# Kernel optimization log

Measured on AMD Instinct MI355X. Metric: run time of the kernel, lower is better.

Reference implementation:

```python
import jax, jax.numpy as jnp
import numpy as np
import math

T, R, H = 3, 5, 8
IN = 256
OUT = 256
DK = OUT // H
N, E, MAXLEN = 30000, 200000, 240
EPS = 1e-5


def _layernorm(x):
    mu = jnp.mean(x, -1, keepdims=True)
    var = jnp.mean((x - mu) ** 2, -1, keepdims=True)
    return (x - mu) / jnp.sqrt(var + EPS)


def _rte_table():
    # fixed sinusoid table from RelTemporalEncoding (non-trainable)
    pos = np.arange(MAXLEN, dtype=np.float32)[:, None]
    div = np.exp(np.arange(0, IN, 2, dtype=np.float32) * -(math.log(10000.0) / IN))
    emb = np.zeros((MAXLEN, IN), dtype=np.float32)
    emb[:, 0::2] = np.sin(pos * div) / math.sqrt(IN)
    emb[:, 1::2] = np.cos(pos * div) / math.sqrt(IN)
    return jnp.asarray(emb)


def setup_inputs():
    key = jax.random.key(0)
    ks = jax.random.split(key, 16)
    g = lambda k, shape, s: jax.random.normal(k, shape, jnp.float32) * s
    inp = {}
    inp['node_inp'] = g(ks[0], (N, IN), 1.0)
    inp['Wk'] = g(ks[1], (T, IN, OUT), 0.02)
    inp['bk'] = jnp.zeros((T, OUT), jnp.float32)
    inp['Wq'] = g(ks[2], (T, IN, OUT), 0.02)
    inp['bq'] = jnp.zeros((T, OUT), jnp.float32)
    inp['Wv'] = g(ks[3], (T, IN, OUT), 0.02)
    inp['bv'] = jnp.zeros((T, OUT), jnp.float32)
    inp['Wa'] = g(ks[4], (T, OUT, OUT), 0.02)
    inp['ba'] = jnp.zeros((T, OUT), jnp.float32)
    inp['ln_g'] = jnp.ones((T, OUT), jnp.float32)
    inp['ln_b'] = jnp.zeros((T, OUT), jnp.float32)
    inp['rel_pri'] = jnp.ones((R, H), jnp.float32)
    inp['rel_att'] = g(ks[5], (R, H, DK, DK), 1.0 / math.sqrt(DK))
    inp['rel_msg'] = g(ks[6], (R, H, DK, DK), 1.0 / math.sqrt(DK))
    inp['skip'] = jnp.ones((T,), jnp.float32)
    inp['rte_W'] = g(ks[7], (IN, IN), 0.02)
    inp['rte_b'] = jnp.zeros((IN,), jnp.float32)
    inp['rte_emb'] = _rte_table()
    inp['node_type'] = jax.random.randint(ks[8], (N,), 0, T)
    inp['edge_index'] = jax.random.randint(ks[9], (2, E), 0, N)
    inp['edge_type'] = jax.random.randint(ks[10], (E,), 0, R)
    inp['edge_time'] = jax.random.randint(ks[11], (E,), 0, MAXLEN)
    return inp


def _forward(node_inp, Wk, bk, Wq, bq, Wv, bv, Wa, ba, ln_g, ln_b,
             rel_pri, rel_att, rel_msg, skip, rte_W, rte_b, rte_emb,
             node_type, edge_index, edge_type, edge_time):
    src, dst = edge_index[0], edge_index[1]  # j (source), i (target)
    nidx = jnp.arange(N)
    # per-type node projections, then pick each node's own type row
    q_node = (jnp.einsum('ni,tio->tno', node_inp, Wq) + bq[:, None, :])[node_type, nidx]
    k_node = (jnp.einsum('ni,tio->tno', node_inp, Wk) + bk[:, None, :])[node_type, nidx]
    v_node = (jnp.einsum('ni,tio->tno', node_inp, Wv) + bv[:, None, :])[node_type, nidx]
    # k_linear(x + rte) = k_linear(x) + rte @ Wk  -> precompute tiny [T, MAXLEN, OUT] tables
    rte_vec = rte_emb @ rte_W.T + rte_b           # [MAXLEN, IN], lin(emb(t))
    rte_k = jnp.einsum('mi,tio->tmo', rte_vec, Wk)
    rte_v = jnp.einsum('mi,tio->tmo', rte_vec, Wv)
    st = node_type[src]
    k_e = (k_node[src] + rte_k[st, edge_time]).reshape(E, H, DK)
    v_e = (v_node[src] + rte_v[st, edge_time]).reshape(E, H, DK)
    q_e = q_node[dst].reshape(E, H, DK)
    # relation-specific bilinear transforms (static small loop over R)
    k_t = jnp.zeros_like(k_e)
    v_t = jnp.zeros_like(v_e)
    for r in range(R):
        m = (edge_type == r)[:, None, None]
        k_t = jnp.where(m, jnp.einsum('ehd,hdf->ehf', k_e, rel_att[r]), k_t)
        v_t = jnp.where(m, jnp.einsum('ehd,hdf->ehf', v_e, rel_msg[r]), v_t)
    logit = jnp.sum(q_e * k_t, -1) * rel_pri[edge_type] / math.sqrt(DK)  # [E, H]
    # segment softmax grouped by target node id
    mx = jax.ops.segment_max(logit, dst, num_segments=N)
    ex = jnp.exp(logit - mx[dst])
    den = jax.ops.segment_sum(ex, dst, num_segments=N)
    att = ex / den[dst]
    msg = (v_t * att[:, :, None]).reshape(E, OUT)
    aggr = jax.ops.segment_sum(msg, dst, num_segments=N)  # [N, OUT]
    # target-specific aggregation, gated skip (dropout is eval no-op)
    trans = (jnp.einsum('no,tof->tnf', aggr, Wa) + ba[:, None, :])[node_type, nidx]
    alpha = jax.nn.sigmoid(skip)[node_type][:, None]
    mixed = trans * alpha + node_inp * (1.0 - alpha)
    return _layernorm(mixed) * ln_g[node_type] + ln_b[node_type]


def reference(node_inp, node_type, edge_index, edge_type, edge_time,
              Wk, bk, Wq, bq, Wv, bv, Wa, ba, ln_g, ln_b,
              rel_pri, rel_att, rel_msg, skip, rte_W, rte_b, rte_emb):
    return _forward(node_inp, Wk, bk, Wq, bq, Wv, bv, Wa, ba, ln_g, ln_b,
                    rel_pri, rel_att, rel_msg, skip, rte_W, rte_b, rte_emb,
                    node_type, edge_index, edge_type, edge_time)
```

## Files before the change

kernel.cpp:

```cpp
#include <hip/hip_runtime.h>
#include <hip/hip_bf16.h>
#include <math.h>

#define NN 30000
#define NE 200000
#define NT 3
#define NR 5
#define NH 8
#define DIM 256
#define ML 240
#define EPSF 1e-5f

typedef __attribute__((ext_vector_type(8))) short short8v;
typedef __attribute__((ext_vector_type(4))) float f32x4;

__device__ __forceinline__ unsigned fkey(float f){
    unsigned b = __float_as_uint(f);
    return (b & 0x80000000u) ? ~b : (b | 0x80000000u);
}
__device__ __forceinline__ float funkey(unsigned u){
    return __uint_as_float((u & 0x80000000u) ? (u & 0x7fffffffu) : ~u);
}
__device__ __forceinline__ unsigned short f2bf(float f){
    unsigned b = __float_as_uint(f);
    unsigned r = (b + 0x7FFFu + ((b >> 16) & 1u)) >> 16;
    return (unsigned short)r;
}

__global__ void k_cvt(const float* __restrict__ in, unsigned short* __restrict__ out){
    int idx = blockIdx.x*256 + threadIdx.x;
    const float4* s = reinterpret_cast<const float4*>(in + (size_t)idx*8);
    float4 a = s[0], b = s[1];
    unsigned short t[8];
    t[0]=f2bf(a.x); t[1]=f2bf(a.y); t[2]=f2bf(a.z); t[3]=f2bf(a.w);
    t[4]=f2bf(b.x); t[5]=f2bf(b.y); t[6]=f2bf(b.z); t[7]=f2bf(b.w);
    *reinterpret_cast<uint4*>(out + (size_t)idx*8) = *reinterpret_cast<uint4*>(t);
}

__global__ __launch_bounds__(256) void k_cvt_w(const float* __restrict__ W,
                                               unsigned short* __restrict__ Wt){
    __shared__ float S[64][65];
    int t = blockIdx.z;
    int i0 = blockIdx.x * 64, o0 = blockIdx.y * 64;
    int th = threadIdx.x;
    int r = th >> 2, c0 = (th & 3) * 16;
    const float* src = W + (size_t)t*65536 + (size_t)(i0 + r)*256 + o0 + c0;
    #pragma unroll
    for (int j = 0; j < 16; j += 4){
        float4 v = *reinterpret_cast<const float4*>(src + j);
        S[r][c0 + j + 0] = v.x; S[r][c0 + j + 1] = v.y;
        S[r][c0 + j + 2] = v.z; S[r][c0 + j + 3] = v.w;
    }
    __syncthreads();
    unsigned short tmp[16];
    #pragma unroll
    for (int j = 0; j < 16; j++) tmp[j] = f2bf(S[c0 + j][r]);
    unsigned short* dst = Wt + (size_t)t*65536 + (size_t)(o0 + r)*256 + i0 + c0;
    *reinterpret_cast<uint4*>(dst)     = *reinterpret_cast<uint4*>(tmp);
    *reinterpret_cast<uint4*>(dst + 8) = *reinterpret_cast<uint4*>(tmp + 8);
}

__global__ void k_rtevec(const float* __restrict__ emb, const float* __restrict__ W,
                         const float* __restrict__ b, float* __restrict__ out){
    __shared__ float se[DIM];
    int m = blockIdx.x, i = threadIdx.x;
    se[i] = emb[m*DIM + i];
    __syncthreads();
    const float* wr = W + i*DIM;
    float acc = 0.f;
    #pragma unroll 8
    for (int j = 0; j < DIM; j += 4){
        float4 w = *reinterpret_cast<const float4*>(wr + j);
        acc += se[j]*w.x + se[j+1]*w.y + se[j+2]*w.z + se[j+3]*w.w;
    }
    out[m*DIM + i] = acc + b[i];
}

__global__ void k_rtekv(const float* __restrict__ rvec, const float* __restrict__ Wk,
                        const float* __restrict__ Wv, float* __restrict__ rk,
                        float* __restrict__ rv){
    __shared__ float sv[DIM];
    int m = blockIdx.x, t = blockIdx.y, o = threadIdx.x;
    sv[o] = rvec[m*DIM + o];
    __syncthreads();
    const float* wk = Wk + (size_t)t*DIM*DIM;
    const float* wv = Wv + (size_t)t*DIM*DIM;
    float ak = 0.f, av = 0.f;
    #pragma unroll 4
    for (int i = 0; i < DIM; i++){
        float s = sv[i];
        ak += s * wk[i*DIM + o];
        av += s * wv[i*DIM + o];
    }
    rk[(t*ML+m)*DIM + o] = ak;
    rv[(t*ML+m)*DIM + o] = av;
}

__global__ void k_bucket(const int* __restrict__ ntype, const int* __restrict__ etype,
                         int* __restrict__ ncnt, int* __restrict__ nlist,
                         int* __restrict__ ecnt, int* __restrict__ elist){
    __shared__ int lc[8];
    __shared__ int lb[8];
    int tid = threadIdx.x;
    if (tid < 8) lc[tid] = 0;
    __syncthreads();
    int idx = blockIdx.x*256 + tid;
    int key = -1, lpos = 0;
    if (idx < NN){
        key = ntype[idx];
        lpos = atomicAdd(&lc[key], 1);
    } else if (idx < NN + NE){
        key = NT + etype[idx - NN];
        lpos = atomicAdd(&lc[key], 1);
    }
    __syncthreads();
    if (tid < 8 && lc[tid] > 0){
        lb[tid] = atomicAdd(tid < NT ? &ncnt[tid] : &ecnt[tid - NT], lc[tid]);
    }
    __syncthreads();
    if (idx < NN){
        nlist[key*NN + lb[key] + lpos] = idx;
    } else if (idx < NN + NE){
        elist[(key - NT)*NE + lb[key] + lpos] = idx - NN;
    }
}

__global__ __launch_bounds__(256) void k_projM(const unsigned short* __restrict__ Xb,
        const int* __restrict__ nlist, const int* __restrict__ ncnt,
        const unsigned short* __restrict__ Wt, const float* __restrict__ bias,
        float* __restrict__ Y){
    __shared__ unsigned short As[128*40];
    __shared__ unsigned short Bs[128*40];
    int t = blockIdx.z;
    int cnt = ncnt[t];
    int m0 = blockIdx.x * 128;
    if (m0 >= cnt) return;
    int o0 = blockIdx.y * 128;
    int th = threadIdx.x;
    const unsigned short* Wtt = Wt + (size_t)t*65536;

    int srow = th >> 1, shalf = th & 1;
    int arow = m0 + srow;
    int anode = (arow < cnt) ? nlist[t*NN + arow] : nlist[t*NN];
    const unsigned short* agp = Xb + (size_t)anode*256 + shalf*16;
    const unsigned short* bgp = Wtt + (size_t)(o0 + srow)*256 + shalf*16;
    uint4* alp = reinterpret_cast<uint4*>(&As[srow*40 + shalf*16]);
    uint4* blp = reinterpret_cast<uint4*>(&Bs[srow*40 + shalf*16]);

    int l = th & 63, w = th >> 6;
    int wm = w >> 1, wn = w & 1;
    int lrow = l & 15, kc = l >> 4;

    f32x4 acc[4][4];
    #pragma unroll
    for (int i = 0; i < 4; i++)
        #pragma unroll
        for (int j = 0; j < 4; j++) acc[i][j] = (f32x4){0.f,0.f,0.f,0.f};

    for (int k0 = 0; k0 < 256; k0 += 32){
        uint4 ga0 = *reinterpret_cast<const uint4*>(agp + k0);
        uint4 ga1 = *reinterpret_cast<const uint4*>(agp + k0 + 8);
        uint4 gb0 = *reinterpret_cast<const uint4*>(bgp + k0);
        uint4 gb1 = *reinterpret_cast<const uint4*>(bgp + k0 + 8);
        __syncthreads();
        alp[0] = ga0; alp[1] = ga1;
        blp[0] = gb0; blp[1] = gb1;
        __syncthreads();
        short8v a[4], b[4];
        #pragma unroll
        for (int mi = 0; mi < 4; mi++)
            a[mi] = *reinterpret_cast<const short8v*>(&As[(wm*64 + mi*16 + lrow)*40 + kc*8]);
        #pragma unroll
        for (int ni = 0; ni < 4; ni++)
            b[ni] = *reinterpret_cast<const short8v*>(&Bs[(wn*64 + ni*16 + lrow)*40 + kc*8]);
        #pragma unroll
        for (int mi = 0; mi < 4; mi++)
            #pragma unroll
            for (int ni = 0; ni < 4; ni++)
                acc[mi][ni] = __builtin_amdgcn_mfma_f32_16x16x32_bf16(a[mi], b[ni], acc[mi][ni], 0, 0, 0);
    }

    float bv[4];
    #pragma unroll
    for (int ni = 0; ni < 4; ni++)
        bv[ni] = bias[t*256 + o0 + wn*64 + ni*16 + (l & 15)];
    #pragma unroll
    for (int mi = 0; mi < 4; mi++){
        #pragma unroll
        for (int j = 0; j < 4; j++){
            int grow = m0 + wm*64 + mi*16 + (l >> 4)*4 + j;
            if (grow < cnt){
                int node = nlist[t*NN + grow];
                float* yp = Y + (size_t)node*256 + o0 + wn*64 + (l & 15);
                #pragma unroll
                for (int ni = 0; ni < 4; ni++)
                    yp[ni*16] = acc[mi][ni][j] + bv[ni];
            }
        }
    }
}

__global__ __launch_bounds__(256) void k_passA(const float* __restrict__ qn,
        const float* __restrict__ kn, const float* __restrict__ rk,
        const int* __restrict__ elist, const int* __restrict__ ecnt,
        const int* __restrict__ esrc, const int* __restrict__ edst,
        const int* __restrict__ etime, const int* __restrict__ ntype,
        const float* __restrict__ rel_att, const float* __restrict__ rel_pri,
        float* __restrict__ logit, unsigned* __restrict__ mx){
    __shared__ int s_src[64], s_dst[64], s_tm[64], s_st[64], s_eid[64];
    __shared__ float ke[64][36], qe[64][36];
    int r = blockIdx.y;
    int cnt = ecnt[r];
    int e0 = blockIdx.x * 64;
    if (e0 >= cnt) return;
    int nE = min(64, cnt - e0);
    int tid = threadIdx.x;
    if (tid < 64){
        int e = elist[r*NE + e0 + (tid < nE ? tid : 0)];
        int sj = esrc[e];
        s_eid[tid] = e; s_src[tid] = sj; s_dst[tid] = edst[e];
        s_tm[tid] = etime[e]; s_st[tid] = ntype[sj];
    }
    __syncthreads();
    int f = tid & 31, mg = tid >> 5;
    const float inv = 0.17677669529663687f;
    for (int h = 0; h < NH; h++){
        #pragma unroll
        for (int u = 0; u < 2; u++){
            int fi = tid + u*256;
            int m = fi >> 3, c4 = (fi & 7) * 4;
            float4 kv = *reinterpret_cast<const float4*>(kn + (size_t)s_src[m]*DIM + h*32 + c4);
            float4 rvv = *reinterpret_cast<const float4*>(rk + (size_t)(s_st[m]*ML + s_tm[m])*DIM + h*32 + c4);
            float4 qv = *reinterpret_cast<const float4*>(qn + (size_t)s_dst[m]*DIM + h*32 + c4);
            kv.x += rvv.x; kv.y += rvv.y; kv.z += rvv.z; kv.w += rvv.w;
            *reinterpret_cast<float4*>(&ke[m][c4]) = kv;
            *reinterpret_cast<float4*>(&qe[m][c4]) = qv;
        }
        __syncthreads();
        float rf[32];
        const float* relb = rel_att + (size_t)(r*NH + h)*1024;
        #pragma unroll
        for (int d = 0; d < 32; d++) rf[d] = relb[d*32 + f];
        float pri = rel_pri[r*NH + h] * inv;
        #pragma unroll
        for (int mi = 0; mi < 8; mi++){
            int m = mg*8 + mi;
            float acc = 0.f;
            #pragma unroll
            for (int d4 = 0; d4 < 8; d4++){
                float4 k4 = *reinterpret_cast<const float4*>(&ke[m][d4*4]);
                acc += k4.x*rf[d4*4] + k4.y*rf[d4*4+1] + k4.z*rf[d4*4+2] + k4.w*rf[d4*4+3];
            }
            float v = acc * qe[m][f];
            v += __shfl_xor(v, 1);
            v += __shfl_xor(v, 2);
            v += __shfl_xor(v, 4);
            v += __shfl_xor(v, 8);
            v += __shfl_xor(v, 16);
            if (f == 0 && m < nE){
                float lv = v * pri;
                logit[(size_t)s_eid[m]*NH + h] = lv;
                atomicMax(&mx[s_dst[m]*NH + h], fkey(lv));
            }
        }
        __syncthreads();
    }
}

__global__ __launch_bounds__(256) void k_passB(const float* __restrict__ vn,
        const float* __restrict__ rv, const int* __restrict__ elist,
        const int* __restrict__ ecnt, const int* __restrict__ esrc,
        const int* __restrict__ edst, const int* __restrict__ etime,
        const int* __restrict__ ntype, const float* __restrict__ rel_msg,
        const float* __restrict__ logit, const unsigned* __restrict__ mx,
        float* __restrict__ den, float* __restrict__ aggr){
    __shared__ int s_src[64], s_dst[64], s_tm[64], s_st[64], s_eid[64];
    __shared__ float ve[64][36];
    int r = blockIdx.y;
    int cnt = ecnt[r];
    int e0 = blockIdx.x * 64;
    if (e0 >= cnt) return;
    int nE = min(64, cnt - e0);
    int tid = threadIdx.x;
    if (tid < 64){
        int e = elist[r*NE + e0 + (tid < nE ? tid : 0)];
        int sj = esrc[e];
        s_eid[tid] = e; s_src[tid] = sj; s_dst[tid] = edst[e];
        s_tm[tid] = etime[e]; s_st[tid] = ntype[sj];
    }
    __syncthreads();
    int f = tid & 31, mg = tid >> 5;
    for (int h = 0; h < NH; h++){
        #pragma unroll
        for (int u = 0; u < 2; u++){
            int fi = tid + u*256;
            int m = fi >> 3, c4 = (fi & 7) * 4;
            float4 vv = *reinterpret_cast<const float4*>(vn + (size_t)s_src[m]*DIM + h*32 + c4);
            float4 rr = *reinterpret_cast<const float4*>(rv + (size_t)(s_st[m]*ML + s_tm[m])*DIM + h*32 + c4);
            vv.x += rr.x; vv.y += rr.y; vv.z += rr.z; vv.w += rr.w;
            *reinterpret_cast<float4*>(&ve[m][c4]) = vv;
        }
        __syncthreads();
        float rf[32];
        const float* relb = rel_msg + (size_t)(r*NH + h)*1024;
        #pragma unroll
        for (int d = 0; d < 32; d++) rf[d] = relb[d*32 + f];
        #pragma unroll
        for (int mi = 0; mi < 8; mi++){
            int m = mg*8 + mi;
            float acc = 0.f;
            #pragma unroll
            for (int d4 = 0; d4 < 8; d4++){
                float4 v4 = *reinterpret_cast<const float4*>(&ve[m][d4*4]);
                acc += v4.x*rf[d4*4] + v4.y*rf[d4*4+1] + v4.z*rf[d4*4+2] + v4.w*rf[d4*4+3];
            }
            if (m < nE){
                float lg = logit[(size_t)s_eid[m]*NH + h];
                float mv = funkey(mx[s_dst[m]*NH + h]);
                float ex = __expf(lg - mv);
                atomicAdd(&aggr[(size_t)s_dst[m]*DIM + h*32 + f], acc*ex);
                if (f == 0) atomicAdd(&den[s_dst[m]*NH + h], ex);
            }
        }
        __syncthreads();
    }
}

__global__ void k_aggdiv(float* __restrict__ aggr, const float* __restrict__ den){
    int idx = blockIdx.x*256 + threadIdx.x;
    int n = idx >> 8, c = idx & 255;
    float d = den[n*NH + (c >> 5)];
    if (d > 0.f) aggr[idx] /= d;
}

__global__ __launch_bounds__(256) void k_epi(const float* __restrict__ trans,
        const float* __restrict__ x, const int* __restrict__ ntype,
        const float* __restrict__ skip, const float* __restrict__ g,
        const float* __restrict__ b, float* __restrict__ out){
    __shared__ float r1[4], r2[4];
    int n = blockIdx.x, c = threadIdx.x;
    int t = ntype[n];
    float alpha = 1.f / (1.f + expf(-skip[t]));
    float mixed = trans[(size_t)n*DIM + c]*alpha + x[(size_t)n*DIM + c]*(1.f - alpha);
    float s = mixed, q = mixed*mixed;
    #pragma unroll
    for (int off = 32; off >= 1; off >>= 1){
        s += __shfl_down(s, off);
        q += __shfl_down(q, off);
    }
    int w = c >> 6;
    if ((c & 63) == 0){ r1[w] = s; r2[w] = q; }
    __syncthreads();
    float S  = r1[0]+r1[1]+r1[2]+r1[3];
    float S2 = r2[0]+r2[1]+r2[2]+r2[3];
    float mu = S * (1.f/DIM);
    float var = S2 * (1.f/DIM) - mu*mu;
    out[(size_t)n*DIM + c] = (mixed - mu) * rsqrtf(var + EPSF) * g[t*DIM + c] + b[t*DIM + c];
}

extern "C" void kernel_launch(void* const* d_in, const int* in_sizes, int n_in,
                              void* d_out, int out_size, void* d_ws, size_t ws_size,
                              hipStream_t stream){
    const float* node_inp = (const float*)d_in[0];
    const float* Wk  = (const float*)d_in[1];
    const float* bk  = (const float*)d_in[2];
    const float* Wq  = (const float*)d_in[3];
    const float* bq  = (const float*)d_in[4];
    const float* Wv  = (const float*)d_in[5];
    const float* bv  = (const float*)d_in[6];
    const float* Wa  = (const float*)d_in[7];
    const float* ba  = (const float*)d_in[8];
    const float* ln_g = (const float*)d_in[9];
    const float* ln_b = (const float*)d_in[10];
    const float* rel_pri = (const float*)d_in[11];
    const float* rel_att = (const float*)d_in[12];
    const float* rel_msg = (const float*)d_in[13];
    const float* skip  = (const float*)d_in[14];
    const float* rte_W = (const float*)d_in[15];
    const float* rte_b = (const float*)d_in[16];
    const float* rte_emb = (const float*)d_in[17];
    const int* ntype = (const int*)d_in[18];
    const int* eidx  = (const int*)d_in[19];
    const int* etype = (const int*)d_in[20];
    const int* etime = (const int*)d_in[21];
    const int* esrc = eidx;
    const int* edst = eidx + NE;

    float* ws = (float*)d_ws;
    size_t o_aggr = 0;
    size_t o_mx   = o_aggr + (size_t)NN*DIM;
    size_t o_den  = o_mx   + (size_t)NN*NH;
    size_t o_cnt  = o_den  + (size_t)NN*NH;
    size_t zeroEnd= o_cnt  + 16;
    size_t o_q    = zeroEnd + 16;
    size_t o_k    = o_q    + (size_t)NN*DIM;
    size_t o_rvec = o_k    + (size_t)NN*DIM;
    size_t o_rk   = o_rvec + (size_t)ML*DIM;
    size_t o_rv   = o_rk   + (size_t)NT*ML*DIM;
    size_t o_logit= o_rv   + (size_t)NT*ML*DIM;
    size_t o_nlist= o_logit+ (size_t)NE*NH;
    size_t o_elist= o_nlist+ (size_t)NT*NN;

    float* aggr = ws + o_aggr;
    unsigned* mx = (unsigned*)(ws + o_mx);
    float* den = ws + o_den;
    int* ncnt = (int*)(ws + o_cnt);
    int* ecnt = ncnt + 8;
    float* qn = ws + o_q;
    float* kn = ws + o_k;
    float* rvec = ws + o_rvec;
    float* rk = ws + o_rk;
    float* rv = ws + o_rv;
    float* logit = ws + o_logit;
    int* nlist = (int*)(ws + o_nlist);
    int* elist = (int*)(ws + o_elist);
    float* vn = qn;
    float* trans = qn;
    float* out = (float*)d_out;

    unsigned short* xb  = (unsigned short*)d_out;
    unsigned short* wtb = (unsigned short*)((float*)d_out + (size_t)NN*DIM/2);
    unsigned short* wtq = wtb;
    unsigned short* wtk = wtb + 1*(size_t)NT*DIM*DIM;
    unsigned short* wtv = wtb + 2*(size_t)NT*DIM*DIM;
    unsigned short* wta = wtb + 3*(size_t)NT*DIM*DIM;
    unsigned short* aggr_bf = (unsigned short*)kn;

    hipMemsetAsync(d_ws, 0, zeroEnd * sizeof(float), stream);
    k_cvt<<<NN*DIM/(8*256), 256, 0, stream>>>(node_inp, xb);
    dim3 wgrid(4, 4, NT);
    k_cvt_w<<<wgrid, 256, 0, stream>>>(Wq, wtq);
    k_cvt_w<<<wgrid, 256, 0, stream>>>(Wk, wtk);
    k_cvt_w<<<wgrid, 256, 0, stream>>>(Wv, wtv);
    k_cvt_w<<<wgrid, 256, 0, stream>>>(Wa, wta);
    k_rtevec<<<ML, 256, 0, stream>>>(rte_emb, rte_W, rte_b, rvec);
    k_rtekv<<<dim3(ML, NT), 256, 0, stream>>>(rvec, Wk, Wv, rk, rv);
    k_bucket<<<(NN+NE+255)/256, 256, 0, stream>>>(ntype, etype, ncnt, nlist, ecnt, elist);

    dim3 pgrid((NN+127)/128, 2, NT);
    k_projM<<<pgrid, 256, 0, stream>>>(xb, nlist, ncnt, wtq, bq, qn);
    k_projM<<<pgrid, 256, 0, stream>>>(xb, nlist, ncnt, wtk, bk, kn);
    dim3 egrid((NE+63)/64, NR);
    k_passA<<<egrid, 256, 0, stream>>>(qn, kn, rk, elist, ecnt, esrc, edst, etime, ntype,
                                       rel_att, rel_pri, logit, mx);
    k_projM<<<pgrid, 256, 0, stream>>>(xb, nlist, ncnt, wtv, bv, vn);
    k_passB<<<egrid, 256, 0, stream>>>(vn, rv, elist, ecnt, esrc, edst, etime, ntype,
                                       rel_msg, logit, mx, den, aggr);
    k_aggdiv<<<(NN*DIM)/256, 256, 0, stream>>>(aggr, den);
    k_cvt<<<NN*DIM/(8*256), 256, 0, stream>>>(aggr, aggr_bf);
    k_projM<<<pgrid, 256, 0, stream>>>(aggr_bf, nlist, ncnt, wta, ba, trans);
    k_epi<<<NN, 256, 0, stream>>>(trans, node_inp, ntype, skip, ln_g, ln_b, out);
}
```

Before: 582.0 us.

## Replace edge-bucketed two-pass attention with destination-CSR online-softmax per node

Edges are now sorted into a CSR by destination node with a degree count, scan and scatter. A single per-node attention kernel (one wavefront per target) does the work of the two edge passes. It folds rel_att into the query and applies rel_msg once after aggregation, per relation, and uses an online softmax. This removes the global atomics for max, denominator and aggregate, the logit buffer, and the separate divide and convert kernels. Q/K/V and the RTE tables are stored as bf16 to halve gather traffic, at some precision cost and with load imbalance from skewed node degrees.

```diff
diff --git a/kernel.cpp b/kernel.cpp
--- a/kernel.cpp
+++ b/kernel.cpp
@@ -14,17 +14,13 @@
 typedef __attribute__((ext_vector_type(8))) short short8v;
 typedef __attribute__((ext_vector_type(4))) float f32x4;
 
-__device__ __forceinline__ unsigned fkey(float f){
-    unsigned b = __float_as_uint(f);
-    return (b & 0x80000000u) ? ~b : (b | 0x80000000u);
-}
-__device__ __forceinline__ float funkey(unsigned u){
-    return __uint_as_float((u & 0x80000000u) ? (u & 0x7fffffffu) : ~u);
-}
 __device__ __forceinline__ unsigned short f2bf(float f){
     unsigned b = __float_as_uint(f);
     unsigned r = (b + 0x7FFFu + ((b >> 16) & 1u)) >> 16;
     return (unsigned short)r;
+}
+__device__ __forceinline__ float bf2f(unsigned short u){
+    return __uint_as_float((unsigned)u << 16);
 }
 
 __global__ void k_cvt(const float* __restrict__ in, unsigned short* __restrict__ out){
@@ -77,8 +73,8 @@
 }
 
 __global__ void k_rtekv(const float* __restrict__ rvec, const float* __restrict__ Wk,
-                        const float* __restrict__ Wv, float* __restrict__ rk,
-                        float* __restrict__ rv){
+                        const float* __restrict__ Wv, unsigned short* __restrict__ rkb,
+                        unsigned short* __restrict__ rvb){
     __shared__ float sv[DIM];
     int m = blockIdx.x, t = blockIdx.y, o = threadIdx.x;
     sv[o] = rvec[m*DIM + o];
@@ -92,17 +88,17 @@
         ak += s * wk[i*DIM + o];
         av += s * wv[i*DIM + o];
     }
-    rk[(t*ML+m)*DIM + o] = ak;
-    rv[(t*ML+m)*DIM + o] = av;
-}
-
-__global__ void k_bucket(const int* __restrict__ ntype, const int* __restrict__ etype,
+    rkb[(t*ML+m)*DIM + o] = f2bf(ak);
+    rvb[(t*ML+m)*DIM + o] = f2bf(av);
+}
+
+__global__ void k_bucket(const int* __restrict__ ntype, const int* __restrict__ edst,
                          int* __restrict__ ncnt, int* __restrict__ nlist,
-                         int* __restrict__ ecnt, int* __restrict__ elist){
-    __shared__ int lc[8];
-    __shared__ int lb[8];
+                         int* __restrict__ deg){
+    __shared__ int lc[4];
+    __shared__ int lb[4];
     int tid = threadIdx.x;
-    if (tid < 8) lc[tid] = 0;
+    if (tid < 4) lc[tid] = 0;
     __syncthreads();
     int idx = blockIdx.x*256 + tid;
     int key = -1, lpos = 0;
@@ -110,25 +106,70 @@
         key = ntype[idx];
         lpos = atomicAdd(&lc[key], 1);
     } else if (idx < NN + NE){
-        key = NT + etype[idx - NN];
-        lpos = atomicAdd(&lc[key], 1);
-    }
-    __syncthreads();
-    if (tid < 8 && lc[tid] > 0){
-        lb[tid] = atomicAdd(tid < NT ? &ncnt[tid] : &ecnt[tid - NT], lc[tid]);
-    }
-    __syncthreads();
-    if (idx < NN){
-        nlist[key*NN + lb[key] + lpos] = idx;
-    } else if (idx < NN + NE){
-        elist[(key - NT)*NE + lb[key] + lpos] = idx - NN;
-    }
-}
-
+        atomicAdd(&deg[edst[idx - NN]], 1);
+    }
+    __syncthreads();
+    if (tid < 3 && lc[tid] > 0) lb[tid] = atomicAdd(&ncnt[tid], lc[tid]);
+    __syncthreads();
+    if (idx < NN) nlist[key*NN + lb[key] + lpos] = idx;
+}
+
+__global__ __launch_bounds__(1024) void k_scan(const int* __restrict__ deg,
+                                               int* __restrict__ off){
+    __shared__ int wsum[16];
+    int t = threadIdx.x;
+    int base = t * 32;
+    int loc[32];
+    int s = 0;
+    #pragma unroll
+    for (int i = 0; i < 32; i++){
+        int idx = base + i;
+        int v = (idx < NN) ? deg[idx] : 0;
+        loc[i] = s;
+        s += v;
+    }
+    int lane = t & 63, w = t >> 6;
+    int sc = s;
+    #pragma unroll
+    for (int d = 1; d < 64; d <<= 1){
+        int o = __shfl_up(sc, d);
+        if (lane >= d) sc += o;
+    }
+    if (lane == 63) wsum[w] = sc;
+    __syncthreads();
+    if (t == 0){
+        int a = 0;
+        #pragma unroll
+        for (int i = 0; i < 16; i++){ int v = wsum[i]; wsum[i] = a; a += v; }
+    }
+    __syncthreads();
+    int tex = (sc - s) + wsum[w];
+    #pragma unroll
+    for (int i = 0; i < 32; i++){
+        int idx = base + i;
+        if (idx <= NN) off[idx] = tex + loc[i];
+    }
+}
+
+__global__ void k_scatter(const int* __restrict__ esrc, const int* __restrict__ edst,
+                          const int* __restrict__ etype, const int* __restrict__ etime,
+                          const int* __restrict__ ntype, const int* __restrict__ off,
+                          int* __restrict__ cur, uint2* __restrict__ csr){
+    int e = blockIdx.x*256 + threadIdx.x;
+    if (e >= NE) return;
+    int d = edst[e];
+    int p = atomicAdd(&cur[d], 1);
+    int src = esrc[e];
+    int st = ntype[src];
+    unsigned meta = ((unsigned)(st*ML + etime[e]) << 3) | (unsigned)etype[e];
+    csr[off[d] + p] = make_uint2((unsigned)src, meta);
+}
+
+template<int BF16OUT>
 __global__ __launch_bounds__(256) void k_projM(const unsigned short* __restrict__ Xb,
         const int* __restrict__ nlist, const int* __restrict__ ncnt,
         const unsigned short* __restrict__ Wt, const float* __restrict__ bias,
-        float* __restrict__ Y){
+        float* __restrict__ Yf, unsigned short* __restrict__ Yb){
     __shared__ unsigned short As[128*40];
     __shared__ unsigned short Bs[128*40];
     int t = blockIdx.z;
@@ -191,146 +232,160 @@
             int grow = m0 + wm*64 + mi*16 + (l >> 4)*4 + j;
             if (grow < cnt){
                 int node = nlist[t*NN + grow];
-                float* yp = Y + (size_t)node*256 + o0 + wn*64 + (l & 15);
-                #pragma unroll
-                for (int ni = 0; ni < 4; ni++)
-                    yp[ni*16] = acc[mi][ni][j] + bv[ni];
+                size_t cb = (size_t)node*256 + o0 + wn*64 + (l & 15);
+                if (BF16OUT){
+                    #pragma unroll
+                    for (int ni = 0; ni < 4; ni++)
+                        Yb[cb + ni*16] = f2bf(acc[mi][ni][j] + bv[ni]);
+                } else {
+                    #pragma unroll
+                    for (int ni = 0; ni < 4; ni++)
+                        Yf[cb + ni*16] = acc[mi][ni][j] + bv[ni];
+                }
             }
         }
     }
 }
 
-__global__ __launch_bounds__(256) void k_passA(const float* __restrict__ qn,
-        const float* __restrict__ kn, const float* __restrict__ rk,
-        const int* __restrict__ elist, const int* __restrict__ ecnt,
-        const int* __restrict__ esrc, const int* __restrict__ edst,
-        const int* __restrict__ etime, const int* __restrict__ ntype,
-        const float* __restrict__ rel_att, const float* __restrict__ rel_pri,
-        float* __restrict__ logit, unsigned* __restrict__ mx){
-    __shared__ int s_src[64], s_dst[64], s_tm[64], s_st[64], s_eid[64];
-    __shared__ float ke[64][36], qe[64][36];
-    int r = blockIdx.y;
-    int cnt = ecnt[r];
-    int e0 = blockIdx.x * 64;
-    if (e0 >= cnt) return;
-    int nE = min(64, cnt - e0);
-    int tid = threadIdx.x;
-    if (tid < 64){
-        int e = elist[r*NE + e0 + (tid < nE ? tid : 0)];
-        int sj = esrc[e];
-        s_eid[tid] = e; s_src[tid] = sj; s_dst[tid] = edst[e];
-        s_tm[tid] = etime[e]; s_st[tid] = ntype[sj];
-    }
-    __syncthreads();
-    int f = tid & 31, mg = tid >> 5;
-    const float inv = 0.17677669529663687f;
-    for (int h = 0; h < NH; h++){
-        #pragma unroll
-        for (int u = 0; u < 2; u++){
-            int fi = tid + u*256;
-            int m = fi >> 3, c4 = (fi & 7) * 4;
-            float4 kv = *reinterpret_cast<const float4*>(kn + (size_t)s_src[m]*DIM + h*32 + c4);
-            float4 rvv = *reinterpret_cast<const float4*>(rk + (size_t)(s_st[m]*ML + s_tm[m])*DIM + h*32 + c4);
-            float4 qv = *reinterpret_cast<const float4*>(qn + (size_t)s_dst[m]*DIM + h*32 + c4);
-            kv.x += rvv.x; kv.y += rvv.y; kv.z += rvv.z; kv.w += rvv.w;
-            *reinterpret_cast<float4*>(&ke[m][c4]) = kv;
-            *reinterpret_cast<float4*>(&qe[m][c4]) = qv;
-        }
-        __syncthreads();
-        float rf[32];
-        const float* relb = rel_att + (size_t)(r*NH + h)*1024;
-        #pragma unroll
-        for (int d = 0; d < 32; d++) rf[d] = relb[d*32 + f];
-        float pri = rel_pri[r*NH + h] * inv;
-        #pragma unroll
-        for (int mi = 0; mi < 8; mi++){
-            int m = mg*8 + mi;
-            float acc = 0.f;
+__global__ __launch_bounds__(256) void k_attn(
+        const unsigned short* __restrict__ qb, const unsigned short* __restrict__ kb,
+        const unsigned short* __restrict__ vb, const unsigned short* __restrict__ rkb,
+        const unsigned short* __restrict__ rvb, const int* __restrict__ off,
+        const uint2* __restrict__ csr, const float* __restrict__ rel_att,
+        const float* __restrict__ rel_msg, const float* __restrict__ rel_pri,
+        unsigned short* __restrict__ ab){
+    int wv = (blockIdx.x << 2) + (threadIdx.x >> 6);
+    int l = threadIdx.x & 63;
+    int h = l >> 3, j = l & 7;
+    int c0 = h*32 + j*4;
+
+    int eb = off[wv], ee = off[wv + 1];
+    if (eb == ee){
+        if (true){
+            ushort4 z = {0,0,0,0};
+            *reinterpret_cast<ushort4*>(ab + (size_t)wv*DIM + c0) = z;
+        }
+        return;
+    }
+
+    float prl[NR];
+    #pragma unroll
+    for (int r = 0; r < NR; r++) prl[r] = rel_pri[r*NH + h] * 0.17677669529663687f;
+
+    float q4[4];
+    {
+        ushort4 qq = *reinterpret_cast<const ushort4*>(qb + (size_t)wv*DIM + c0);
+        q4[0] = bf2f(qq.x); q4[1] = bf2f(qq.y); q4[2] = bf2f(qq.z); q4[3] = bf2f(qq.w);
+    }
+
+    float qt[NR][4];
+    #pragma unroll
+    for (int r = 0; r < NR; r++){ qt[r][0]=0.f; qt[r][1]=0.f; qt[r][2]=0.f; qt[r][3]=0.f; }
+    #pragma unroll
+    for (int s = 0; s < 8; s++){
+        int jj = (j + s) & 7;
+        int srcl = (l & 0x38) | jj;
+        float qs0 = __shfl(q4[0], srcl), qs1 = __shfl(q4[1], srcl);
+        float qs2 = __shfl(q4[2], srcl), qs3 = __shfl(q4[3], srcl);
+        #pragma unroll
+        for (int r = 0; r < NR; r++){
+            const float* Mb = rel_att + (size_t)((r*NH + h)*32)*32;
             #pragma unroll
-            for (int d4 = 0; d4 < 8; d4++){
-                float4 k4 = *reinterpret_cast<const float4*>(&ke[m][d4*4]);
-                acc += k4.x*rf[d4*4] + k4.y*rf[d4*4+1] + k4.z*rf[d4*4+2] + k4.w*rf[d4*4+3];
+            for (int dd = 0; dd < 4; dd++){
+                float4 mr = *reinterpret_cast<const float4*>(Mb + (4*j + dd)*32 + 4*jj);
+                qt[r][dd] += qs0*mr.x + qs1*mr.y + qs2*mr.z + qs3*mr.w;
             }
-            float v = acc * qe[m][f];
-            v += __shfl_xor(v, 1);
-            v += __shfl_xor(v, 2);
-            v += __shfl_xor(v, 4);
-            v += __shfl_xor(v, 8);
-            v += __shfl_xor(v, 16);
-            if (f == 0 && m < nE){
-                float lv = v * pri;
-                logit[(size_t)s_eid[m]*NH + h] = lv;
-                atomicMax(&mx[s_dst[m]*NH + h], fkey(lv));
-            }
-        }
-        __syncthreads();
-    }
-}
-
-__global__ __launch_bounds__(256) void k_passB(const float* __restrict__ vn,
-        const float* __restrict__ rv, const int* __restrict__ elist,
-        const int* __restrict__ ecnt, const int* __restrict__ esrc,
-        const int* __restrict__ edst, const int* __restrict__ etime,
-        const int* __restrict__ ntype, const float* __restrict__ rel_msg,
-        const float* __restrict__ logit, const unsigned* __restrict__ mx,
-        float* __restrict__ den, float* __restrict__ aggr){
-    __shared__ int s_src[64], s_dst[64], s_tm[64], s_st[64], s_eid[64];
-    __shared__ float ve[64][36];
-    int r = blockIdx.y;
-    int cnt = ecnt[r];
-    int e0 = blockIdx.x * 64;
-    if (e0 >= cnt) return;
-    int nE = min(64, cnt - e0);
-    int tid = threadIdx.x;
-    if (tid < 64){
-        int e = elist[r*NE + e0 + (tid < nE ? tid : 0)];
-        int sj = esrc[e];
-        s_eid[tid] = e; s_src[tid] = sj; s_dst[tid] = edst[e];
-        s_tm[tid] = etime[e]; s_st[tid] = ntype[sj];
-    }
-    __syncthreads();
-    int f = tid & 31, mg = tid >> 5;
-    for (int h = 0; h < NH; h++){
-        #pragma unroll
-        for (int u = 0; u < 2; u++){
-            int fi = tid + u*256;
-            int m = fi >> 3, c4 = (fi & 7) * 4;
-            float4 vv = *reinterpret_cast<const float4*>(vn + (size_t)s_src[m]*DIM + h*32 + c4);
-            float4 rr = *reinterpret_cast<const float4*>(rv + (size_t)(s_st[m]*ML + s_tm[m])*DIM + h*32 + c4);
-            vv.x += rr.x; vv.y += rr.y; vv.z += rr.z; vv.w += rr.w;
-            *reinterpret_cast<float4*>(&ve[m][c4]) = vv;
-        }
-        __syncthreads();
-        float rf[32];
-        const float* relb = rel_msg + (size_t)(r*NH + h)*1024;
-        #pragma unroll
-        for (int d = 0; d < 32; d++) rf[d] = relb[d*32 + f];
-        #pragma unroll
-        for (int mi = 0; mi < 8; mi++){
-            int m = mg*8 + mi;
-            float acc = 0.f;
-            #pragma unroll
-            for (int d4 = 0; d4 < 8; d4++){
-                float4 v4 = *reinterpret_cast<const float4*>(&ve[m][d4*4]);
-                acc += v4.x*rf[d4*4] + v4.y*rf[d4*4+1] + v4.z*rf[d4*4+2] + v4.w*rf[d4*4+3];
-            }
-            if (m < nE){
-                float lg = logit[(size_t)s_eid[m]*NH + h];
-                float mv = funkey(mx[s_dst[m]*NH + h]);
-                float ex = __expf(lg - mv);
-                atomicAdd(&aggr[(size_t)s_dst[m]*DIM + h*32 + f], acc*ex);
-                if (f == 0) atomicAdd(&den[s_dst[m]*NH + h], ex);
-            }
-        }
-        __syncthreads();
-    }
-}
-
-__global__ void k_aggdiv(float* __restrict__ aggr, const float* __restrict__ den){
-    int idx = blockIdx.x*256 + threadIdx.x;
-    int n = idx >> 8, c = idx & 255;
-    float d = den[n*NH + (c >> 5)];
-    if (d > 0.f) aggr[idx] /= d;
+        }
+    }
+
+    float m_run = -1e30f, den = 0.f;
+    float acc[NR][4];
+    #pragma unroll
+    for (int r = 0; r < NR; r++){ acc[r][0]=0.f; acc[r][1]=0.f; acc[r][2]=0.f; acc[r][3]=0.f; }
+
+    for (int p = eb; p < ee; p++){
+        uint2 em = csr[p];
+        int src = (int)em.x;
+        int r = (int)(em.y & 7u);
+        int rr = (int)(em.y >> 3);
+        float k4[4];
+        {
+            ushort4 kk = *reinterpret_cast<const ushort4*>(kb + (size_t)src*DIM + c0);
+            ushort4 rk = *reinterpret_cast<const ushort4*>(rkb + (size_t)rr*DIM + c0);
+            k4[0] = bf2f(kk.x) + bf2f(rk.x); k4[1] = bf2f(kk.y) + bf2f(rk.y);
+            k4[2] = bf2f(kk.z) + bf2f(rk.z); k4[3] = bf2f(kk.w) + bf2f(rk.w);
+        }
+        float dt;
+        switch (r){
+            case 0: dt = qt[0][0]*k4[0]+qt[0][1]*k4[1]+qt[0][2]*k4[2]+qt[0][3]*k4[3]; break;
+            case 1: dt = qt[1][0]*k4[0]+qt[1][1]*k4[1]+qt[1][2]*k4[2]+qt[1][3]*k4[3]; break;
+            case 2: dt = qt[2][0]*k4[0]+qt[2][1]*k4[1]+qt[2][2]*k4[2]+qt[2][3]*k4[3]; break;
+            case 3: dt = qt[3][0]*k4[0]+qt[3][1]*k4[1]+qt[3][2]*k4[2]+qt[3][3]*k4[3]; break;
+            default:dt = qt[4][0]*k4[0]+qt[4][1]*k4[1]+qt[4][2]*k4[2]+qt[4][3]*k4[3]; break;
+        }
+        dt += __shfl_xor(dt, 1);
+        dt += __shfl_xor(dt, 2);
+        dt += __shfl_xor(dt, 4);
+        float lg = dt * prl[r];
+        switch (r){
+            case 0: lg = dt * prl[0]; break;
+            case 1: lg = dt * prl[1]; break;
+            case 2: lg = dt * prl[2]; break;
+            case 3: lg = dt * prl[3]; break;
+            default:lg = dt * prl[4]; break;
+        }
+        float mnew = fmaxf(m_run, lg);
+        float fac = __expf(m_run - mnew);
+        float ex  = __expf(lg - mnew);
+        den = den*fac + ex;
+        #pragma unroll
+        for (int r2 = 0; r2 < NR; r2++){
+            acc[r2][0]*=fac; acc[r2][1]*=fac; acc[r2][2]*=fac; acc[r2][3]*=fac;
+        }
+        m_run = mnew;
+        float v4[4];
+        {
+            ushort4 vv = *reinterpret_cast<const ushort4*>(vb + (size_t)src*DIM + c0);
+            ushort4 rv = *reinterpret_cast<const ushort4*>(rvb + (size_t)rr*DIM + c0);
+            v4[0] = bf2f(vv.x) + bf2f(rv.x); v4[1] = bf2f(vv.y) + bf2f(rv.y);
+            v4[2] = bf2f(vv.z) + bf2f(rv.z); v4[3] = bf2f(vv.w) + bf2f(rv.w);
+        }
+        switch (r){
+            case 0: acc[0][0]+=ex*v4[0]; acc[0][1]+=ex*v4[1]; acc[0][2]+=ex*v4[2]; acc[0][3]+=ex*v4[3]; break;
+            case 1: acc[1][0]+=ex*v4[0]; acc[1][1]+=ex*v4[1]; acc[1][2]+=ex*v4[2]; acc[1][3]+=ex*v4[3]; break;
+            case 2: acc[2][0]+=ex*v4[0]; acc[2][1]+=ex*v4[1]; acc[2][2]+=ex*v4[2]; acc[2][3]+=ex*v4[3]; break;
+            case 3: acc[3][0]+=ex*v4[0]; acc[3][1]+=ex*v4[1]; acc[3][2]+=ex*v4[2]; acc[3][3]+=ex*v4[3]; break;
+            default:acc[4][0]+=ex*v4[0]; acc[4][1]+=ex*v4[1]; acc[4][2]+=ex*v4[2]; acc[4][3]+=ex*v4[3]; break;
+        }
+    }
+
+    float o[4] = {0.f, 0.f, 0.f, 0.f};
+    #pragma unroll
+    for (int s = 0; s < 8; s++){
+        int jj = (j + s) & 7;
+        int srcl = (l & 0x38) | jj;
+        #pragma unroll
+        for (int r = 0; r < NR; r++){
+            float a0 = __shfl(acc[r][0], srcl);
+            float a1 = __shfl(acc[r][1], srcl);
+            float a2 = __shfl(acc[r][2], srcl);
+            float a3 = __shfl(acc[r][3], srcl);
+            const float* Mb = rel_msg + (size_t)((r*NH + h)*32)*32 + 4*j;
+            float4 m0 = *reinterpret_cast<const float4*>(Mb + (size_t)(4*jj + 0)*32);
+            float4 m1 = *reinterpret_cast<const float4*>(Mb + (size_t)(4*jj + 1)*32);
+            float4 m2 = *reinterpret_cast<const float4*>(Mb + (size_t)(4*jj + 2)*32);
+            float4 m3 = *reinterpret_cast<const float4*>(Mb + (size_t)(4*jj + 3)*32);
+            o[0] += a0*m0.x + a1*m1.x + a2*m2.x + a3*m3.x;
+            o[1] += a0*m0.y + a1*m1.y + a2*m2.y + a3*m3.y;
+            o[2] += a0*m0.z + a1*m1.z + a2*m2.z + a3*m3.z;
+            o[3] += a0*m0.w + a1*m1.w + a2*m2.w + a3*m3.w;
+        }
+    }
+    float inv_den = (den > 0.f) ? (1.f / den) : 0.f;
+    ushort4 res;
+    res.x = f2bf(o[0]*inv_den); res.y = f2bf(o[1]*inv_den);
+    res.z = f2bf(o[2]*inv_den); res.w = f2bf(o[3]*inv_den);
+    *reinterpret_cast<ushort4*>(ab + (size_t)wv*DIM + c0) = res;
 }
 
 __global__ __launch_bounds__(256) void k_epi(const float* __restrict__ trans,
@@ -386,47 +441,31 @@
     const int* esrc = eidx;
     const int* edst = eidx + NE;
 
-    float* ws = (float*)d_ws;
-    size_t o_aggr = 0;
-    size_t o_mx   = o_aggr + (size_t)NN*DIM;
-    size_t o_den  = o_mx   + (size_t)NN*NH;
-    size_t o_cnt  = o_den  + (size_t)NN*NH;
-    size_t zeroEnd= o_cnt  + 16;
-    size_t o_q    = zeroEnd + 16;
-    size_t o_k    = o_q    + (size_t)NN*DIM;
-    size_t o_rvec = o_k    + (size_t)NN*DIM;
-    size_t o_rk   = o_rvec + (size_t)ML*DIM;
-    size_t o_rv   = o_rk   + (size_t)NT*ML*DIM;
-    size_t o_logit= o_rv   + (size_t)NT*ML*DIM;
-    size_t o_nlist= o_logit+ (size_t)NE*NH;
-    size_t o_elist= o_nlist+ (size_t)NT*NN;
-
-    float* aggr = ws + o_aggr;
-    unsigned* mx = (unsigned*)(ws + o_mx);
-    float* den = ws + o_den;
-    int* ncnt = (int*)(ws + o_cnt);
-    int* ecnt = ncnt + 8;
-    float* qn = ws + o_q;
-    float* kn = ws + o_k;
-    float* rvec = ws + o_rvec;
-    float* rk = ws + o_rk;
-    float* rv = ws + o_rv;
-    float* logit = ws + o_logit;
-    int* nlist = (int*)(ws + o_nlist);
-    int* elist = (int*)(ws + o_elist);
-    float* vn = qn;
-    float* trans = qn;
+    char* base = (char*)d_ws;
+    unsigned short* qb  = (unsigned short*)(base);
+    unsigned short* kb  = (unsigned short*)(base + 15360000);
+    unsigned short* vb  = (unsigned short*)(base + 30720000);
+    unsigned short* ab  = (unsigned short*)(base + 46080000);
+    unsigned short* rkb = (unsigned short*)(base + 61440000);
+    unsigned short* rvb = (unsigned short*)(base + 61808640);
+    float* rvec         = (float*)(base + 62177280);
+    int* ncnt           = (int*)(base + 62423040);
+    int* deg            = (int*)(base + 62423104);
+    int* cur            = (int*)(base + 62543104);
+    int* off            = (int*)(base + 62663104);
+    uint2* csr          = (uint2*)(base + 62783168);
+    int* nlist          = (int*)(base + 64383168);
+    float* trans        = (float*)kb;
     float* out = (float*)d_out;
 
     unsigned short* xb  = (unsigned short*)d_out;
-    unsigned short* wtb = (unsigned short*)((float*)d_out + (size_t)NN*DIM/2);
+    unsigned short* wtb = (unsigned short*)((char*)d_out + 15360000);
     unsigned short* wtq = wtb;
     unsigned short* wtk = wtb + 1*(size_t)NT*DIM*DIM;
     unsigned short* wtv = wtb + 2*(size_t)NT*DIM*DIM;
     unsigned short* wta = wtb + 3*(size_t)NT*DIM*DIM;
-    unsigned short* aggr_bf = (unsigned short*)kn;
-
-    hipMemsetAsync(d_ws, 0, zeroEnd * sizeof(float), stream);
+
+    hipMemsetAsync((void*)ncnt, 0, 64 + 120000 + 120000, stream);
     k_cvt<<<NN*DIM/(8*256), 256, 0, stream>>>(node_inp, xb);
     dim3 wgrid(4, 4, NT);
     k_cvt_w<<<wgrid, 256, 0, stream>>>(Wq, wtq);
@@ -434,20 +473,17 @@
     k_cvt_w<<<wgrid, 256, 0, stream>>>(Wv, wtv);
     k_cvt_w<<<wgrid, 256, 0, stream>>>(Wa, wta);
     k_rtevec<<<ML, 256, 0, stream>>>(rte_emb, rte_W, rte_b, rvec);
-    k_rtekv<<<dim3(ML, NT), 256, 0, stream>>>(rvec, Wk, Wv, rk, rv);
-    k_bucket<<<(NN+NE+255)/256, 256, 0, stream>>>(ntype, etype, ncnt, nlist, ecnt, elist);
+    k_rtekv<<<dim3(ML, NT), 256, 0, stream>>>(rvec, Wk, Wv, rkb, rvb);
+    k_bucket<<<(NN+NE+255)/256, 256, 0, stream>>>(ntype, edst, ncnt, nlist, deg);
+    k_scan<<<1, 1024, 0, stream>>>(deg, off);
+    k_scatter<<<(NE+255)/256, 256, 0, stream>>>(esrc, edst, etype, etime, ntype, off, cur, csr);
 
     dim3 pgrid((NN+127)/128, 2, NT);
-    k_projM<<<pgrid, 256, 0, stream>>>(xb, nlist, ncnt, wtq, bq, qn);
-    k_projM<<<pgrid, 256, 0, stream>>>(xb, nlist, ncnt, wtk, bk, kn);
-    dim3 egrid((NE+63)/64, NR);
-    k_passA<<<egrid, 256, 0, stream>>>(qn, kn, rk, elist, ecnt, esrc, edst, etime, ntype,
-                                       rel_att, rel_pri, logit, mx);
-    k_projM<<<pgrid, 256, 0, stream>>>(xb, nlist, ncnt, wtv, bv, vn);
-    k_passB<<<egrid, 256, 0, stream>>>(vn, rv, elist, ecnt, esrc, edst, etime, ntype,
-                                       rel_msg, logit, mx, den, aggr);
-    k_aggdiv<<<(NN*DIM)/256, 256, 0, stream>>>(aggr, den);
-    k_cvt<<<NN*DIM/(8*256), 256, 0, stream>>>(aggr, aggr_bf);
-    k_projM<<<pgrid, 256, 0, stream>>>(aggr_bf, nlist, ncnt, wta, ba, trans);
+    k_projM<1><<<pgrid, 256, 0, stream>>>(xb, nlist, ncnt, wtq, bq, nullptr, qb);
+    k_projM<1><<<pgrid, 256, 0, stream>>>(xb, nlist, ncnt, wtk, bk, nullptr, kb);
+    k_projM<1><<<pgrid, 256, 0, stream>>>(xb, nlist, ncnt, wtv, bv, nullptr, vb);
+    k_attn<<<NN/4, 256, 0, stream>>>(qb, kb, vb, rkb, rvb, off, csr,
+                                     rel_att, rel_msg, rel_pri, ab);
+    k_projM<0><<<pgrid, 256, 0, stream>>>(ab, nlist, ncnt, wta, ba, trans, nullptr);
     k_epi<<<NN, 256, 0, stream>>>(trans, node_inp, ntype, skip, ln_g, ln_b, out);
 }
```

New measurement: 2.147 ms. +268.8%, slower.
